# Performance work log

Hardware: AMD Instinct MI355X
Metric: run time of the kernel (lower is better)

Reference implementation:

```python
import jax, jax.numpy as jnp
import numpy as np

NUM_HEADS = 8
DIM_HEAD = 32


def setup_inputs() -> dict:
    key = jax.random.key(0)
    k1, k2, k3 = jax.random.split(key, 3)
    dim = 256
    inner = NUM_HEADS * DIM_HEAD  # 256
    x = jax.random.normal(k1, (2, dim, 32, 32, 32), dtype=jnp.float32)
    # Conv1d(kernel_size=1, bias=False) weights == plain matrices [out_ch, in_ch]
    w_qkv = jax.random.normal(k2, (inner * 3, dim), dtype=jnp.float32) * 0.02
    w_out = jax.random.normal(k3, (dim, inner), dtype=jnp.float32) * 0.02
    return {"x": x, "w_qkv": w_qkv, "w_out": w_out}


def reference(x, w_qkv, w_out):
    b, c, h, w, d = x.shape
    n = h * w * d
    x_flat = x.reshape(b, c, n)
    # 1x1 conv == channel matmul: [b, 3*inner, n]
    qkv = jnp.einsum('oc,bcn->bon', w_qkv, x_flat)
    q, k, v = jnp.split(qkv, 3, axis=1)

    def to_heads(t):  # [b, inner, n] -> [b, H, n, Dh]
        return t.reshape(b, NUM_HEADS, DIM_HEAD, n).transpose(0, 1, 3, 2)

    q = jax.nn.softmax(to_heads(q), axis=-1)   # softmax over dim_head
    k = jax.nn.softmax(to_heads(k), axis=-2)   # softmax over tokens n
    v = to_heads(v)
    # context: [b, H, Dh, Dh]
    context = jnp.einsum('bhnd,bhne->bhde', k, v)
    attn_out = jnp.einsum('bhnd,bhde->bhne', q, context)  # [b, H, n, Dh]
    attn_out = attn_out.transpose(0, 1, 3, 2).reshape(b, NUM_HEADS * DIM_HEAD, n)
    out = jnp.einsum('oi,bin->bon', w_out, attn_out)  # to_out 1x1 conv (dropout=0)
    return out.reshape(b, c, h, w, d)
```

## Files before the change

### kernel.cpp

```cpp
#include <hip/hip_runtime.h>

#define NTOK 32768

typedef __attribute__((ext_vector_type(8))) short  bf16x8;
typedef __attribute__((ext_vector_type(8))) unsigned short u16x8;
typedef __attribute__((ext_vector_type(4))) float  f32x4;

__device__ __forceinline__ unsigned short f32_to_bf16(float f) {
    unsigned int u = __float_as_uint(f);
    u += 0x7FFFu + ((u >> 16) & 1u);
    return (unsigned short)(u >> 16);
}
__device__ __forceinline__ float bf16_to_f32(unsigned short h) {
    return __uint_as_float(((unsigned int)h) << 16);
}

template <typename BT, typename CT, int MCHUNKS, bool QSOFT>
__global__ __launch_bounds__(256) void gemm_bstat(
    const unsigned short* __restrict__ A, const BT* __restrict__ B,
    CT* __restrict__ C, long sA, long sB, long sC)
{
    const int bz = blockIdx.y;
    A += (long)bz * sA; B += (long)bz * sB; C += (long)bz * sC;
    const int col0 = blockIdx.x * 128;

    __shared__ unsigned short Bs[128 * 256];

    const int t = threadIdx.x;
    const int wave = t >> 6, lane = t & 63;
    const int wm = wave >> 1, wn = wave & 1;
    const int m16 = lane & 15, quad = lane >> 4;

    {
        const int n = t & 127;
        const int kg0 = (t >> 7) * 16;
        const int key = n & 7;
        const BT* bcol = B + col0 + n;
        #pragma unroll
        for (int g = 0; g < 16; ++g) {
            const int kg = kg0 + g;
            unsigned short tmp[8];
            #pragma unroll
            for (int i = 0; i < 8; ++i) {
                BT v = bcol[(size_t)(kg * 8 + i) * NTOK];
                if constexpr (sizeof(BT) == 4) tmp[i] = f32_to_bf16((float)v);
                else                           tmp[i] = (unsigned short)v;
            }
            *(u16x8*)&Bs[n * 256 + ((kg ^ key) * 8)] = *(const u16x8*)tmp;
        }
    }
    __syncthreads();

    const int swk = m16 & 7;

    for (int mc = 0; mc < MCHUNKS; ++mc) {
        const int m0 = mc * 128;
        f32x4 acc[4][4] = {};

        const unsigned short* Abase = A + (size_t)(m0 + wm * 64 + m16) * 256 + quad * 8;

        bf16x8 af_cur[4], af_nxt[4];
        #pragma unroll
        for (int mt = 0; mt < 4; ++mt)
            af_cur[mt] = *(const bf16x8*)&Abase[(size_t)mt * 16 * 256];

        #pragma unroll
        for (int kk = 0; kk < 8; ++kk) {
            if (kk < 7) {
                #pragma unroll
                for (int mt = 0; mt < 4; ++mt)
                    af_nxt[mt] = *(const bf16x8*)
                        &Abase[(size_t)mt * 16 * 256 + (kk + 1) * 32];
            }

            bf16x8 bf[4];
            #pragma unroll
            for (int nt = 0; nt < 4; ++nt) {
                const int col = wn * 64 + nt * 16 + m16;
                bf[nt] = *(const bf16x8*)&Bs[col * 256 + (((kk * 4 + quad) ^ swk) * 8)];
            }
            #pragma unroll
            for (int mt = 0; mt < 4; ++mt)
                #pragma unroll
                for (int nt = 0; nt < 4; ++nt)
                    acc[mt][nt] = __builtin_amdgcn_mfma_f32_16x16x32_bf16(
                        bf[nt], af_cur[mt], acc[mt][nt], 0, 0, 0);

            #pragma unroll
            for (int mt = 0; mt < 4; ++mt) af_cur[mt] = af_nxt[mt];
        }

        if (QSOFT && m0 < 256) {
            #pragma unroll
            for (int hj = 0; hj < 2; ++hj) {
                #pragma unroll
                for (int nt = 0; nt < 4; ++nt) {
                    #pragma unroll
                    for (int r = 0; r < 4; ++r) {
                        float mx = fmaxf(acc[hj * 2][nt][r], acc[hj * 2 + 1][nt][r]);
                        mx = fmaxf(mx, __shfl_xor(mx, 1, 64));
                        mx = fmaxf(mx, __shfl_xor(mx, 2, 64));
                        mx = fmaxf(mx, __shfl_xor(mx, 4, 64));
                        mx = fmaxf(mx, __shfl_xor(mx, 8, 64));
                        const float e0 = __expf(acc[hj * 2][nt][r] - mx);
                        const float e1 = __expf(acc[hj * 2 + 1][nt][r] - mx);
                        float s = e0 + e1;
                        s += __shfl_xor(s, 1, 64);
                        s += __shfl_xor(s, 2, 64);
                        s += __shfl_xor(s, 4, 64);
                        s += __shfl_xor(s, 8, 64);
                        const float inv = 1.0f / s;
                        acc[hj * 2][nt][r]     = e0 * inv;
                        acc[hj * 2 + 1][nt][r] = e1 * inv;
                    }
                }
            }
        }

        #pragma unroll
        for (int mt = 0; mt < 4; ++mt) {
            const int row = m0 + wm * 64 + mt * 16 + m16;
            #pragma unroll
            for (int nt = 0; nt < 4; ++nt) {
                const int col = col0 + wn * 64 + nt * 16 + quad * 4;
                if constexpr (sizeof(CT) == 4) {
                    *(float4*)&C[(size_t)row * NTOK + col] =
                        *(const float4*)&acc[mt][nt];
                } else {
                    ushort4 o;
                    o.x = f32_to_bf16(acc[mt][nt][0]);
                    o.y = f32_to_bf16(acc[mt][nt][1]);
                    o.z = f32_to_bf16(acc[mt][nt][2]);
                    o.w = f32_to_bf16(acc[mt][nt][3]);
                    *(ushort4*)&C[(size_t)row * NTOK + col] = o;
                }
            }
        }
    }
}

__global__ __launch_bounds__(256) void cast_bf16_kernel(
    const float* __restrict__ src, unsigned short* __restrict__ dst, int n4)
{
    const int i = blockIdx.x * 256 + threadIdx.x;
    if (i < n4) {
        float4 v = ((const float4*)src)[i];
        ushort4 o;
        o.x = f32_to_bf16(v.x); o.y = f32_to_bf16(v.y);
        o.z = f32_to_bf16(v.z); o.w = f32_to_bf16(v.w);
        ((ushort4*)dst)[i] = o;
    }
}

#define CCHUNK 256
__global__ __launch_bounds__(512) void ctx_mfma_kernel(
    const unsigned short* __restrict__ qkv,
    float* __restrict__ num, float* __restrict__ den)
{
    const int b = blockIdx.y;
    const int n0 = blockIdx.x * CCHUNK;
    const int h = threadIdx.x >> 6;
    const int lane = threadIdx.x & 63;
    const int m16 = lane & 15, quad = lane >> 4;

    const unsigned short* kb =
        qkv + ((long)b * 768 + 256 + h * 32 + m16) * (long)NTOK + n0 + quad * 8;
    const unsigned short* vb =
        qkv + ((long)b * 768 + 512 + h * 32 + m16) * (long)NTOK + n0 + quad * 8;

    f32x4 acc[2][2] = {};
    float dp[2] = {0.f, 0.f};

    #pragma unroll
    for (int n = 0; n < CCHUNK; n += 32) {
        bf16x8 af[2], bfv[2];
        #pragma unroll
        for (int dt = 0; dt < 2; ++dt) {
            const u16x8 kr = *(const u16x8*)(kb + (size_t)dt * 16 * NTOK + n);
            unsigned short tmp[8];
            #pragma unroll
            for (int i = 0; i < 8; ++i) {
                const float e = __expf(bf16_to_f32(kr[i]));
                const unsigned short eb = f32_to_bf16(e);
                tmp[i] = eb;
                dp[dt] += bf16_to_f32(eb);
            }
            af[dt] = *(const bf16x8*)tmp;
        }
        #pragma unroll
        for (int et = 0; et < 2; ++et)
            bfv[et] = *(const bf16x8*)(vb + (size_t)et * 16 * NTOK + n);
        #pragma unroll
        for (int dt = 0; dt < 2; ++dt)
            #pragma unroll
            for (int et = 0; et < 2; ++et)
                acc[dt][et] = __builtin_amdgcn_mfma_f32_16x16x32_bf16(
                    af[dt], bfv[et], acc[dt][et], 0, 0, 0);
    }

    float* nbase = num + ((long)(b * 8 + h) * 32) * 32;
    #pragma unroll
    for (int dt = 0; dt < 2; ++dt)
        #pragma unroll
        for (int et = 0; et < 2; ++et)
            #pragma unroll
            for (int r = 0; r < 4; ++r)
                atomicAdd(&nbase[(dt * 16 + quad * 4 + r) * 32 + et * 16 + m16],
                          acc[dt][et][r]);

    #pragma unroll
    for (int dt = 0; dt < 2; ++dt) {
        float s = dp[dt];
        s += __shfl_xor(s, 16, 64);
        s += __shfl_xor(s, 32, 64);
        if (quad == 0)
            atomicAdd(&den[b * 256 + h * 32 + dt * 16 + m16], s);
    }
}

__global__ __launch_bounds__(256) void combine_kernel(
    const float* __restrict__ w_out, const float* __restrict__ num,
    const float* __restrict__ den, unsigned short* __restrict__ W2)
{
    const int tid = blockIdx.x * 256 + threadIdx.x;
    const int b = tid >> 16;
    const int rem = tid & 65535;
    const int o = rem >> 8;
    const int i = rem & 255;
    const int h = i >> 5, d = i & 31;
    const float* wrow = w_out + o * 256 + h * 32;
    const float* nrow = num + (((long)(b * 8 + h) * 32 + d) << 5);
    float s = 0.f;
    #pragma unroll
    for (int e = 0; e < 32; ++e) s += wrow[e] * nrow[e];
    W2[tid] = f32_to_bf16(s / den[b * 256 + h * 32 + d]);
}

extern "C" void kernel_launch(void* const* d_in, const int* in_sizes, int n_in,
                              void* d_out, int out_size, void* d_ws, size_t ws_size,
                              hipStream_t stream)
{
    const float* x     = (const float*)d_in[0];
    const float* w_qkv = (const float*)d_in[1];
    const float* w_out = (const float*)d_in[2];
    float* out = (float*)d_out;

    unsigned short* qkv_bf = (unsigned short*)d_ws;
    const long qkv_elems = 2L * 768 * NTOK;
    unsigned short* wqkv_bf = qkv_bf + qkv_elems;
    unsigned short* W2 = wqkv_bf + 768 * 256;
    float* num  = (float*)(W2 + 2 * 256 * 256);
    float* den  = num + 16384;

    hipMemsetAsync(num, 0, (16384 + 512) * sizeof(float), stream);

    cast_bf16_kernel<<<192, 256, 0, stream>>>(w_qkv, wqkv_bf, 768 * 256 / 4);

    gemm_bstat<float, unsigned short, 6, true><<<dim3(256, 2), 256, 0, stream>>>(
        wqkv_bf, x, qkv_bf, 0L, 256L * NTOK, 768L * NTOK);

    ctx_mfma_kernel<<<dim3(NTOK / CCHUNK, 2), 512, 0, stream>>>(qkv_bf, num, den);

    combine_kernel<<<512, 256, 0, stream>>>(w_out, num, den, W2);

    gemm_bstat<unsigned short, float, 2, false><<<dim3(256, 2), 256, 0, stream>>>(
        W2, qkv_bf, out, 65536L, 768L * NTOK, 256L * NTOK);
}
```

Baseline: 268.7 us.

## Store intermediate qkv in column-strip tiled layout for contiguous access

Changes the bf16 qkv intermediate buffer from row-major [768, NTOK] to strip-tiled [256 strips][768][128], so each 128-token strip is contiguous. The first GEMM writes tiles, the context kernel reads two strips per block, and the output GEMM loads B tiles with a 128-element stride. The goal is less scattered DRAM traffic and TLB pressure from the 64KB row strides. It also adds template parameters to choose tiled or row-major B and C.

Result: no change. 267.8 us (-0.3%).

```diff
diff --git a/kernel.cpp b/kernel.cpp
--- a/kernel.cpp
+++ b/kernel.cpp
@@ -1,6 +1,7 @@
 #include <hip/hip_runtime.h>
 
 #define NTOK 32768
+#define TSTRIP 98304
 
 typedef __attribute__((ext_vector_type(8))) short  bf16x8;
 typedef __attribute__((ext_vector_type(8))) unsigned short u16x8;
@@ -15,14 +16,20 @@
     return __uint_as_float(((unsigned int)h) << 16);
 }
 
-template <typename BT, typename CT, int MCHUNKS, bool QSOFT>
+template <typename BT, typename CT, int MCHUNKS, bool QSOFT, bool BTILED, bool CTILED>
 __global__ __launch_bounds__(256) void gemm_bstat(
     const unsigned short* __restrict__ A, const BT* __restrict__ B,
     CT* __restrict__ C, long sA, long sB, long sC)
 {
     const int bz = blockIdx.y;
     A += (long)bz * sA; B += (long)bz * sB; C += (long)bz * sC;
-    const int col0 = blockIdx.x * 128;
+    const int strip = blockIdx.x;
+    const int col0 = strip * 128;
+
+    const BT* Bbase = BTILED ? B + (size_t)strip * TSTRIP : B + col0;
+    const long bstride = BTILED ? 128 : NTOK;
+    CT* Cbase = CTILED ? C + (size_t)strip * TSTRIP : C + col0;
+    const long cstride = CTILED ? 128 : NTOK;
 
     __shared__ unsigned short Bs[128 * 256];
 
@@ -35,14 +42,14 @@
         const int n = t & 127;
         const int kg0 = (t >> 7) * 16;
         const int key = n & 7;
-        const BT* bcol = B + col0 + n;
+        const BT* bcol = Bbase + n;
         #pragma unroll
         for (int g = 0; g < 16; ++g) {
             const int kg = kg0 + g;
             unsigned short tmp[8];
             #pragma unroll
             for (int i = 0; i < 8; ++i) {
-                BT v = bcol[(size_t)(kg * 8 + i) * NTOK];
+                BT v = bcol[(size_t)(kg * 8 + i) * bstride];
                 if constexpr (sizeof(BT) == 4) tmp[i] = f32_to_bf16((float)v);
                 else                           tmp[i] = (unsigned short)v;
             }
@@ -122,9 +129,9 @@
             const int row = m0 + wm * 64 + mt * 16 + m16;
             #pragma unroll
             for (int nt = 0; nt < 4; ++nt) {
-                const int col = col0 + wn * 64 + nt * 16 + quad * 4;
+                const int col = wn * 64 + nt * 16 + quad * 4;
                 if constexpr (sizeof(CT) == 4) {
-                    *(float4*)&C[(size_t)row * NTOK + col] =
+                    *(float4*)&Cbase[(size_t)row * cstride + col] =
                         *(const float4*)&acc[mt][nt];
                 } else {
                     ushort4 o;
@@ -132,7 +139,7 @@
                     o.y = f32_to_bf16(acc[mt][nt][1]);
                     o.z = f32_to_bf16(acc[mt][nt][2]);
                     o.w = f32_to_bf16(acc[mt][nt][3]);
-                    *(ushort4*)&C[(size_t)row * NTOK + col] = o;
+                    *(ushort4*)&Cbase[(size_t)row * cstride + col] = o;
                 }
             }
         }
@@ -152,50 +159,53 @@
     }
 }
 
-#define CCHUNK 256
 __global__ __launch_bounds__(512) void ctx_mfma_kernel(
     const unsigned short* __restrict__ qkv,
     float* __restrict__ num, float* __restrict__ den)
 {
     const int b = blockIdx.y;
-    const int n0 = blockIdx.x * CCHUNK;
+    const int s0 = blockIdx.x * 2;
     const int h = threadIdx.x >> 6;
     const int lane = threadIdx.x & 63;
     const int m16 = lane & 15, quad = lane >> 4;
 
-    const unsigned short* kb =
-        qkv + ((long)b * 768 + 256 + h * 32 + m16) * (long)NTOK + n0 + quad * 8;
-    const unsigned short* vb =
-        qkv + ((long)b * 768 + 512 + h * 32 + m16) * (long)NTOK + n0 + quad * 8;
+    const unsigned short* base = qkv + (long)b * 768 * NTOK;
 
     f32x4 acc[2][2] = {};
     float dp[2] = {0.f, 0.f};
 
     #pragma unroll
-    for (int n = 0; n < CCHUNK; n += 32) {
-        bf16x8 af[2], bfv[2];
-        #pragma unroll
-        for (int dt = 0; dt < 2; ++dt) {
-            const u16x8 kr = *(const u16x8*)(kb + (size_t)dt * 16 * NTOK + n);
-            unsigned short tmp[8];
-            #pragma unroll
-            for (int i = 0; i < 8; ++i) {
-                const float e = __expf(bf16_to_f32(kr[i]));
-                const unsigned short eb = f32_to_bf16(e);
-                tmp[i] = eb;
-                dp[dt] += bf16_to_f32(eb);
-            }
-            af[dt] = *(const bf16x8*)tmp;
-        }
-        #pragma unroll
-        for (int et = 0; et < 2; ++et)
-            bfv[et] = *(const bf16x8*)(vb + (size_t)et * 16 * NTOK + n);
-        #pragma unroll
-        for (int dt = 0; dt < 2; ++dt)
+    for (int st = 0; st < 2; ++st) {
+        const unsigned short* tile = base + (size_t)(s0 + st) * TSTRIP;
+        const unsigned short* kp = tile + (256 + h * 32 + m16) * 128 + quad * 8;
+        const unsigned short* vp = tile + (512 + h * 32 + m16) * 128 + quad * 8;
+        #pragma unroll
+        for (int kg = 0; kg < 4; ++kg) {
+            const int off = kg * 32;
+            bf16x8 af[2], bfv[2];
+            #pragma unroll
+            for (int dt = 0; dt < 2; ++dt) {
+                const u16x8 kr = *(const u16x8*)(kp + dt * 2048 + off);
+                unsigned short tmp[8];
+                #pragma unroll
+                for (int i = 0; i < 8; ++i) {
+                    const float e = __expf(bf16_to_f32(kr[i]));
+                    const unsigned short eb = f32_to_bf16(e);
+                    tmp[i] = eb;
+                    dp[dt] += bf16_to_f32(eb);
+                }
+                af[dt] = *(const bf16x8*)tmp;
+            }
             #pragma unroll
             for (int et = 0; et < 2; ++et)
-                acc[dt][et] = __builtin_amdgcn_mfma_f32_16x16x32_bf16(
-                    af[dt], bfv[et], acc[dt][et], 0, 0, 0);
+                bfv[et] = *(const bf16x8*)(vp + et * 2048 + off);
+            #pragma unroll
+            for (int dt = 0; dt < 2; ++dt)
+                #pragma unroll
+                for (int et = 0; et < 2; ++et)
+                    acc[dt][et] = __builtin_amdgcn_mfma_f32_16x16x32_bf16(
+                        af[dt], bfv[et], acc[dt][et], 0, 0, 0);
+        }
     }
 
     float* nbase = num + ((long)(b * 8 + h) * 32) * 32;
@@ -256,13 +266,15 @@
 
     cast_bf16_kernel<<<192, 256, 0, stream>>>(w_qkv, wqkv_bf, 768 * 256 / 4);
 
-    gemm_bstat<float, unsigned short, 6, true><<<dim3(256, 2), 256, 0, stream>>>(
+    gemm_bstat<float, unsigned short, 6, true, false, true>
+        <<<dim3(256, 2), 256, 0, stream>>>(
         wqkv_bf, x, qkv_bf, 0L, 256L * NTOK, 768L * NTOK);
 
-    ctx_mfma_kernel<<<dim3(NTOK / CCHUNK, 2), 512, 0, stream>>>(qkv_bf, num, den);
+    ctx_mfma_kernel<<<dim3(NTOK / 256, 2), 512, 0, stream>>>(qkv_bf, num, den);
 
     combine_kernel<<<512, 256, 0, stream>>>(w_out, num, den, W2);
 
-    gemm_bstat<unsigned short, float, 2, false><<<dim3(256, 2), 256, 0, stream>>>(
+    gemm_bstat<unsigned short, float, 2, false, true, false>
+        <<<dim3(256, 2), 256, 0, stream>>>(
         W2, qkv_bf, out, 65536L, 768L * NTOK, 256L * NTOK);
 }
```
